# Optimization experiments

Hardware: AMD Instinct MI355X
Metric: run time of the kernel (lower is better)

## Reference

```python
import jax, jax.numpy as jnp
import numpy as np

CONTEXT_SIZE = 128
EMBED_DIM = 128
NUM_HEADS = 4
HEAD_SIZE = EMBED_DIM // NUM_HEADS  # 32


def setup_inputs() -> dict:
    key = jax.random.key(0)
    ks = jax.random.split(key, 9)
    B, T, D, H, hd = 4096, 128, EMBED_DIM, NUM_HEADS, HEAD_SIZE
    s = 1.0 / np.sqrt(D)
    return {
        "x": jax.random.normal(ks[0], (B, T, D), dtype=jnp.float32),
        "Wq": jax.random.normal(ks[1], (H, D, hd), dtype=jnp.float32) * s,
        "bq": jnp.zeros((H, hd), dtype=jnp.float32),
        "Wk": jax.random.normal(ks[2], (H, D, hd), dtype=jnp.float32) * s,
        "bk": jnp.zeros((H, hd), dtype=jnp.float32),
        "Wv": jax.random.normal(ks[3], (H, D, hd), dtype=jnp.float32) * s,
        "bv": jnp.zeros((H, hd), dtype=jnp.float32),
        "Wp": jax.random.normal(ks[4], (D, D), dtype=jnp.float32) * s,
        "bp": jnp.zeros((D,), dtype=jnp.float32),
    }


def reference(x, Wq, bq, Wk, bk, Wv, bv, Wp, bp):
    B, T, D = x.shape
    # per-head projections, batched over heads: [B,H,T,hd]
    q = jnp.einsum("btd,hdk->bhtk", x, Wq) + bq[None, :, None, :]
    k = jnp.einsum("btd,hdk->bhtk", x, Wk) + bk[None, :, None, :]
    v = jnp.einsum("btd,hdk->bhtk", x, Wv) + bv[None, :, None, :]
    # NOTE: original scales by context_size**-0.5, not head_size**-0.5
    scale = CONTEXT_SIZE ** (-0.5)
    scores = jnp.einsum("bhqk,bhsk->bhqs", q, k) * scale  # [B,H,T,T]
    causal = jnp.tril(jnp.ones((T, T), dtype=bool))
    scores = jnp.where(causal[None, None, :, :], scores, -jnp.inf)
    attn = jax.nn.softmax(scores, axis=-1)
    out = jnp.einsum("bhqs,bhsk->bhqk", attn, v)  # [B,H,T,hd]
    # concat heads along feature dim (head order matches ModuleList order)
    out = out.transpose(0, 2, 1, 3).reshape(B, T, D)
    # final projection; dropout is identity in eval mode
    return out @ Wp + bp
```

## Files before the change

kernel.cpp:

```cpp
#include <hip/hip_runtime.h>

#define NB 4096
#define T_ 128
#define D_ 128
#define H_ 4
#define HD_ 32

typedef __attribute__((ext_vector_type(8))) short short8;
typedef __attribute__((ext_vector_type(4))) float float4v;

__device__ inline unsigned short f2bf(float f) {
  unsigned int u = __builtin_bit_cast(unsigned int, f);
  u += 0x7fffu + ((u >> 16) & 1u);
  return (unsigned short)(u >> 16);
}


__global__ __launch_bounds__(512, 4) void mha_kernel(
    const float* __restrict__ x,  const float* __restrict__ Wq,
    const float* __restrict__ bq, const float* __restrict__ Wk,
    const float* __restrict__ bk, const float* __restrict__ Wv,
    const float* __restrict__ bv, const float* __restrict__ Wp,
    const float* __restrict__ bp, float* __restrict__ out)
{
  __shared__ __align__(16) unsigned short smem[32000];
  const int tid  = threadIdx.x;
  const int b    = blockIdx.x;
  const int wv_i = tid >> 6;
  const int lane = tid & 63;
  const int quad = lane >> 4;
  const int n16  = lane & 15;

  unsigned short* xs  = smem;
  unsigned short* osw = smem + wv_i * 2176;
  unsigned short* ks  = smem + 17408;
  unsigned short* wt  = smem + 22528;
  unsigned short* Ew  = smem + 26880 + wv_i * 640;
  unsigned short* wpT = smem + 17408;

  const float4* x4 = (const float4*)(x + (size_t)b * 16384);
  #pragma unroll
  for (int i = 0; i < 8; ++i) {
    float4 v = x4[i * 512 + tid];
    int fl = (i * 512 + tid) * 4;
    xs[fl + 0] = f2bf(v.x); xs[fl + 1] = f2bf(v.y);
    xs[fl + 2] = f2bf(v.z); xs[fl + 3] = f2bf(v.w);
  }
  __syncthreads();

  short8 xfrag[4];
  {
    const unsigned short* base = xs + (wv_i * 16 + n16) * 128 + quad * 8;
    #pragma unroll
    for (int kk = 0; kk < 4; ++kk)
      xfrag[kk] = *(const short8*)(base + kk * 32);
  }
  __syncthreads();

  auto stageWT = [&](const float* Wsrc) {
    #pragma unroll
    for (int i = 0; i < 2; ++i) {
      int g4 = tid + i * 512;
      float4 v = ((const float4*)Wsrc)[g4];
      int g = g4 * 4; int d = g >> 5; int e = g & 31;
      wt[(e + 0) * 136 + d] = f2bf(v.x);
      wt[(e + 1) * 136 + d] = f2bf(v.y);
      wt[(e + 2) * 136 + d] = f2bf(v.z);
      wt[(e + 3) * 136 + d] = f2bf(v.w);
    }
  };

  auto projQKV = [&](float4v acc[2]) {
    #pragma unroll
    for (int nt = 0; nt < 2; ++nt) {
      acc[nt] = (float4v)(0.0f);
      #pragma unroll
      for (int kk = 0; kk < 4; ++kk) {
        short8 bfr = *(const short8*)(wt + (nt * 16 + n16) * 136 + kk * 32 + quad * 8);
        acc[nt] = __builtin_amdgcn_mfma_f32_16x16x32_bf16(xfrag[kk], bfr, acc[nt], 0, 0, 0);
      }
    }
  };

  const float LOG2E_SCALE = 0.08838834764831845f * 1.4426950408889634f;

  #pragma unroll 1
  for (int h = 0; h < H_; ++h) {
    __syncthreads();
    stageWT(Wk + h * 4096);
    __syncthreads();
    float4v kacc[2]; projQKV(kacc);
    #pragma unroll
    for (int nt = 0; nt < 2; ++nt) {
      float bias = bk[h * 32 + nt * 16 + n16];
      #pragma unroll
      for (int r = 0; r < 4; ++r)
        ks[(wv_i * 16 + quad * 4 + r) * 40 + nt * 16 + n16] = f2bf(kacc[nt][r] + bias);
    }
    __syncthreads();
    stageWT(Wq + h * 4096);
    __syncthreads();
    float4v qacc[2]; projQKV(qacc);
    #pragma unroll
    for (int nt = 0; nt < 2; ++nt) {
      float bias = bq[h * 32 + nt * 16 + n16];
      #pragma unroll
      for (int r = 0; r < 4; ++r)
        Ew[(quad * 4 + r) * 40 + nt * 16 + n16] = f2bf(qacc[nt][r] + bias);
    }
    short8 qfrag = *(const short8*)(Ew + n16 * 40 + quad * 8);
    __syncthreads();
    stageWT(Wv + h * 4096);
    __syncthreads();
    float4v vacc[2]; projQKV(vacc);
    __syncthreads();
    #pragma unroll
    for (int nt = 0; nt < 2; ++nt) {
      float bias = bv[h * 32 + nt * 16 + n16];
      #pragma unroll
      for (int r = 0; r < 4; ++r)
        wt[(nt * 16 + n16) * 136 + wv_i * 16 + quad * 4 + r] = f2bf(vacc[nt][r] + bias);
    }
    __syncthreads();

    float4v s[8];
    #pragma unroll
    for (int t = 0; t < 8; ++t) {
      if (t <= wv_i) {
        short8 kfr = *(const short8*)(ks + (t * 16 + n16) * 40 + quad * 8);
        float4v acc = __builtin_amdgcn_mfma_f32_16x16x32_bf16(qfrag, kfr, (float4v)(0.0f), 0, 0, 0);
        if (t == wv_i) {
          #pragma unroll
          for (int r = 0; r < 4; ++r)
            if (n16 > quad * 4 + r) acc[r] = -__builtin_inff();
        }
        s[t] = acc;
      }
    }

    float l[4];
    #pragma unroll
    for (int r = 0; r < 4; ++r) {
      float mm = -__builtin_inff();
      #pragma unroll
      for (int t = 0; t < 8; ++t) if (t <= wv_i) mm = fmaxf(mm, s[t][r]);
      #pragma unroll
      for (int off = 8; off >= 1; off >>= 1) mm = fmaxf(mm, __shfl_xor(mm, off, 64));
      float ll = 0.0f;
      #pragma unroll
      for (int t = 0; t < 8; ++t) if (t <= wv_i) {
        float p = exp2f((s[t][r] - mm) * LOG2E_SCALE);
        s[t][r] = p; ll += p;
      }
      #pragma unroll
      for (int off = 8; off >= 1; off >>= 1) ll += __shfl_xor(ll, off, 64);
      l[r] = ll;
    }

    float4v oacc[2] = {(float4v)(0.0f), (float4v)(0.0f)};
    #pragma unroll
    for (int c = 0; c < 4; ++c) {
      if (2 * c <= wv_i) {
        #pragma unroll
        for (int tt = 0; tt < 2; ++tt) {
          int t = 2 * c + tt;
          #pragma unroll
          for (int r = 0; r < 4; ++r)
            Ew[(quad * 4 + r) * 40 + tt * 16 + n16] =
                (t <= wv_i) ? f2bf(s[t][r]) : (unsigned short)0;
        }
        short8 pfrag = *(const short8*)(Ew + n16 * 40 + quad * 8);
        #pragma unroll
        for (int et = 0; et < 2; ++et) {
          short8 vfr = *(const short8*)(wt + (et * 16 + n16) * 136 + c * 32 + quad * 8);
          oacc[et] = __builtin_amdgcn_mfma_f32_16x16x32_bf16(pfrag, vfr, oacc[et], 0, 0, 0);
        }
      }
    }
    #pragma unroll
    for (int et = 0; et < 2; ++et) {
      #pragma unroll
      for (int r = 0; r < 4; ++r)
        osw[(quad * 4 + r) * 136 + h * 32 + et * 16 + n16] = f2bf(oacc[et][r] / l[r]);
    }
  }

  short8 ofrag[4];
  #pragma unroll
  for (int kk = 0; kk < 4; ++kk)
    ofrag[kk] = *(const short8*)(osw + n16 * 136 + kk * 32 + quad * 8);
  float* outb = out + (size_t)b * 16384;

  #pragma unroll 1
  for (int half = 0; half < 2; ++half) {
    __syncthreads();
    #pragma unroll
    for (int i = 0; i < 4; ++i) {
      int g4 = tid + i * 512;
      int g = g4 * 4; int c = g >> 6; int dd = g & 63;
      float4 v = *(const float4*)(Wp + c * 128 + half * 64 + dd);
      wpT[(dd + 0) * 136 + c] = f2bf(v.x);
      wpT[(dd + 1) * 136 + c] = f2bf(v.y);
      wpT[(dd + 2) * 136 + c] = f2bf(v.z);
      wpT[(dd + 3) * 136 + c] = f2bf(v.w);
    }
    __syncthreads();
    #pragma unroll
    for (int nt = 0; nt < 4; ++nt) {
      float4v acc = (float4v)(0.0f);
      #pragma unroll
      for (int kk = 0; kk < 4; ++kk) {
        short8 bfr = *(const short8*)(wpT + (nt * 16 + n16) * 136 + kk * 32 + quad * 8);
        acc = __builtin_amdgcn_mfma_f32_16x16x32_bf16(ofrag[kk], bfr, acc, 0, 0, 0);
      }
      int col = half * 64 + nt * 16 + n16;
      float bias = bp[col];
      #pragma unroll
      for (int r = 0; r < 4; ++r)
        outb[(size_t)(wv_i * 16 + quad * 4 + r) * 128 + col] = acc[r] + bias;
    }
  }
}

extern "C" void kernel_launch(void* const* d_in, const int* in_sizes, int n_in,
                              void* d_out, int out_size, void* d_ws, size_t ws_size,
                              hipStream_t stream) {
  const float* x  = (const float*)d_in[0];
  const float* Wq = (const float*)d_in[1];
  const float* bq = (const float*)d_in[2];
  const float* Wk = (const float*)d_in[3];
  const float* bk = (const float*)d_in[4];
  const float* Wv = (const float*)d_in[5];
  const float* bv = (const float*)d_in[6];
  const float* Wp = (const float*)d_in[7];
  const float* bp = (const float*)d_in[8];
  mha_kernel<<<dim3(NB), dim3(512), 0, stream>>>(
      x, Wq, bq, Wk, bk, Wv, bv, Wp, bp, (float*)d_out);
}
```

Before: 719.7 us.

## Pre-convert weights to bf16 once and read MFMA operands directly from global

A small prep kernel converts and transposes Wq/Wk/Wv/Wp to bf16 in the workspace once per call. The main kernel then loads weight MFMA fragments straight from global/L2 instead of restaging and transposing fp32 weights through LDS in every block. x fragments are loaded directly into registers, and the per-head syncs collapse from five to two. LDS use drops from 64KB to about 29KB, which may allow more blocks per CU, at the cost of an extra launch and uncached-looking global fragment loads.

```diff
diff --git a/kernel.cpp b/kernel.cpp
--- a/kernel.cpp
+++ b/kernel.cpp
@@ -1,12 +1,9 @@
 #include <hip/hip_runtime.h>
 
 #define NB 4096
-#define T_ 128
-#define D_ 128
-#define H_ 4
-#define HD_ 32
 
 typedef __attribute__((ext_vector_type(8))) short short8;
+typedef __attribute__((ext_vector_type(4))) short short4v;
 typedef __attribute__((ext_vector_type(4))) float float4v;
 
 __device__ inline unsigned short f2bf(float f) {
@@ -15,15 +12,32 @@
   return (unsigned short)(u >> 16);
 }
 
+__global__ __launch_bounds__(256) void prep_weights(
+    const float* __restrict__ Wq, const float* __restrict__ Wk,
+    const float* __restrict__ Wv, const float* __restrict__ Wp,
+    unsigned short* __restrict__ ws)
+{
+  int idx = blockIdx.x * 256 + threadIdx.x;
+  if (idx < 49152) {
+    int m = idx >> 14;
+    int r = idx & 16383;
+    int h = r >> 12, e = (r >> 7) & 31, d = r & 127;
+    const float* W = (m == 0) ? Wq : (m == 1) ? Wk : Wv;
+    ws[idx] = f2bf(W[h * 4096 + d * 32 + e]);
+  } else if (idx < 65536) {
+    int r = idx - 49152;
+    int col = r >> 7, d = r & 127;
+    ws[idx] = f2bf(Wp[d * 128 + col]);
+  }
+}
 
 __global__ __launch_bounds__(512, 4) void mha_kernel(
-    const float* __restrict__ x,  const float* __restrict__ Wq,
-    const float* __restrict__ bq, const float* __restrict__ Wk,
-    const float* __restrict__ bk, const float* __restrict__ Wv,
-    const float* __restrict__ bv, const float* __restrict__ Wp,
-    const float* __restrict__ bp, float* __restrict__ out)
+    const float* __restrict__ x, const unsigned short* __restrict__ wbf,
+    const float* __restrict__ bq, const float* __restrict__ bk,
+    const float* __restrict__ bv, const float* __restrict__ bp,
+    float* __restrict__ out)
 {
-  __shared__ __align__(16) unsigned short smem[32000];
+  __shared__ __align__(16) unsigned short smem[14592];
   const int tid  = threadIdx.x;
   const int b    = blockIdx.x;
   const int wv_i = tid >> 6;
@@ -31,65 +45,54 @@
   const int quad = lane >> 4;
   const int n16  = lane & 15;
 
-  unsigned short* xs  = smem;
-  unsigned short* osw = smem + wv_i * 2176;
-  unsigned short* ks  = smem + 17408;
-  unsigned short* wt  = smem + 22528;
-  unsigned short* Ew  = smem + 26880 + wv_i * 640;
-  unsigned short* wpT = smem + 17408;
-
-  const float4* x4 = (const float4*)(x + (size_t)b * 16384);
+  unsigned short* ks = smem;
+  unsigned short* vt = smem + 5120;
+  unsigned short* Ew = smem + 9472 + wv_i * 640;
+
+  const unsigned short* wq  = wbf;
+  const unsigned short* wk  = wbf + 16384;
+  const unsigned short* wvw = wbf + 32768;
+  const unsigned short* wpT = wbf + 49152;
+
+  const float* xrow = x + (size_t)b * 16384 + (wv_i * 16 + n16) * 128 + quad * 8;
+  short8 xfrag[4];
   #pragma unroll
-  for (int i = 0; i < 8; ++i) {
-    float4 v = x4[i * 512 + tid];
-    int fl = (i * 512 + tid) * 4;
-    xs[fl + 0] = f2bf(v.x); xs[fl + 1] = f2bf(v.y);
-    xs[fl + 2] = f2bf(v.z); xs[fl + 3] = f2bf(v.w);
-  }
-  __syncthreads();
-
-  short8 xfrag[4];
-  {
-    const unsigned short* base = xs + (wv_i * 16 + n16) * 128 + quad * 8;
-    #pragma unroll
-    for (int kk = 0; kk < 4; ++kk)
-      xfrag[kk] = *(const short8*)(base + kk * 32);
-  }
-  __syncthreads();
-
-  auto stageWT = [&](const float* Wsrc) {
-    #pragma unroll
-    for (int i = 0; i < 2; ++i) {
-      int g4 = tid + i * 512;
-      float4 v = ((const float4*)Wsrc)[g4];
-      int g = g4 * 4; int d = g >> 5; int e = g & 31;
-      wt[(e + 0) * 136 + d] = f2bf(v.x);
-      wt[(e + 1) * 136 + d] = f2bf(v.y);
-      wt[(e + 2) * 136 + d] = f2bf(v.z);
-      wt[(e + 3) * 136 + d] = f2bf(v.w);
+  for (int kk = 0; kk < 4; ++kk) {
+    float4 a = *(const float4*)(xrow + kk * 32);
+    float4 c = *(const float4*)(xrow + kk * 32 + 4);
+    short8 f;
+    f[0] = (short)f2bf(a.x); f[1] = (short)f2bf(a.y);
+    f[2] = (short)f2bf(a.z); f[3] = (short)f2bf(a.w);
+    f[4] = (short)f2bf(c.x); f[5] = (short)f2bf(c.y);
+    f[6] = (short)f2bf(c.z); f[7] = (short)f2bf(c.w);
+    xfrag[kk] = f;
+  }
+
+  auto projQKV = [&](const unsigned short* wm, float4v acc[2]) {
+    #pragma unroll
+    for (int nt = 0; nt < 2; ++nt) {
+      acc[nt] = (float4v)(0.0f);
+      #pragma unroll
+      for (int kk = 0; kk < 4; ++kk) {
+        short8 bfr = *(const short8*)(wm + (nt * 16 + n16) * 128 + kk * 32 + quad * 8);
+        acc[nt] = __builtin_amdgcn_mfma_f32_16x16x32_bf16(xfrag[kk], bfr, acc[nt], 0, 0, 0);
+      }
     }
   };
 
-  auto projQKV = [&](float4v acc[2]) {
-    #pragma unroll
-    for (int nt = 0; nt < 2; ++nt) {
-      acc[nt] = (float4v)(0.0f);
-      #pragma unroll
-      for (int kk = 0; kk < 4; ++kk) {
-        short8 bfr = *(const short8*)(wt + (nt * 16 + n16) * 136 + kk * 32 + quad * 8);
-        acc[nt] = __builtin_amdgcn_mfma_f32_16x16x32_bf16(xfrag[kk], bfr, acc[nt], 0, 0, 0);
-      }
-    }
-  };
-
   const float LOG2E_SCALE = 0.08838834764831845f * 1.4426950408889634f;
 
+  short8 ofrag0, ofrag1, ofrag2, ofrag3;
+
   #pragma unroll 1
-  for (int h = 0; h < H_; ++h) {
+  for (int h = 0; h < 4; ++h) {
+    float4v kacc[2], qacc[2], vacc[2];
+    projQKV(wk  + h * 4096, kacc);
+    projQKV(wq  + h * 4096, qacc);
+    projQKV(wvw + h * 4096, vacc);
+
     __syncthreads();
-    stageWT(Wk + h * 4096);
-    __syncthreads();
-    float4v kacc[2]; projQKV(kacc);
+
     #pragma unroll
     for (int nt = 0; nt < 2; ++nt) {
       float bias = bk[h * 32 + nt * 16 + n16];
@@ -97,10 +100,14 @@
       for (int r = 0; r < 4; ++r)
         ks[(wv_i * 16 + quad * 4 + r) * 40 + nt * 16 + n16] = f2bf(kacc[nt][r] + bias);
     }
-    __syncthreads();
-    stageWT(Wq + h * 4096);
-    __syncthreads();
-    float4v qacc[2]; projQKV(qacc);
+    #pragma unroll
+    for (int nt = 0; nt < 2; ++nt) {
+      float bias = bv[h * 32 + nt * 16 + n16];
+      short4v p;
+      #pragma unroll
+      for (int r = 0; r < 4; ++r) p[r] = (short)f2bf(vacc[nt][r] + bias);
+      *(short4v*)(vt + (nt * 16 + n16) * 136 + wv_i * 16 + quad * 4) = p;
+    }
     #pragma unroll
     for (int nt = 0; nt < 2; ++nt) {
       float bias = bq[h * 32 + nt * 16 + n16];
@@ -109,18 +116,7 @@
         Ew[(quad * 4 + r) * 40 + nt * 16 + n16] = f2bf(qacc[nt][r] + bias);
     }
     short8 qfrag = *(const short8*)(Ew + n16 * 40 + quad * 8);
-    __syncthreads();
-    stageWT(Wv + h * 4096);
-    __syncthreads();
-    float4v vacc[2]; projQKV(vacc);
-    __syncthreads();
-    #pragma unroll
-    for (int nt = 0; nt < 2; ++nt) {
-      float bias = bv[h * 32 + nt * 16 + n16];
-      #pragma unroll
-      for (int r = 0; r < 4; ++r)
-        wt[(nt * 16 + n16) * 136 + wv_i * 16 + quad * 4 + r] = f2bf(vacc[nt][r] + bias);
-    }
+
     __syncthreads();
 
     float4v s[8];
@@ -172,52 +168,42 @@
         short8 pfrag = *(const short8*)(Ew + n16 * 40 + quad * 8);
         #pragma unroll
         for (int et = 0; et < 2; ++et) {
-          short8 vfr = *(const short8*)(wt + (et * 16 + n16) * 136 + c * 32 + quad * 8);
+          short8 vfr = *(const short8*)(vt + (et * 16 + n16) * 136 + c * 32 + quad * 8);
           oacc[et] = __builtin_amdgcn_mfma_f32_16x16x32_bf16(pfrag, vfr, oacc[et], 0, 0, 0);
         }
       }
     }
+
+    float inv0 = 1.0f / l[0], inv1 = 1.0f / l[1], inv2 = 1.0f / l[2], inv3 = 1.0f / l[3];
     #pragma unroll
     for (int et = 0; et < 2; ++et) {
+      Ew[(quad * 4 + 0) * 40 + et * 16 + n16] = f2bf(oacc[et][0] * inv0);
+      Ew[(quad * 4 + 1) * 40 + et * 16 + n16] = f2bf(oacc[et][1] * inv1);
+      Ew[(quad * 4 + 2) * 40 + et * 16 + n16] = f2bf(oacc[et][2] * inv2);
+      Ew[(quad * 4 + 3) * 40 + et * 16 + n16] = f2bf(oacc[et][3] * inv3);
+    }
+    short8 of = *(const short8*)(Ew + n16 * 40 + quad * 8);
+    if (h == 0) ofrag0 = of; else if (h == 1) ofrag1 = of;
+    else if (h == 2) ofrag2 = of; else ofrag3 = of;
+  }
+
+  float* outb = out + (size_t)b * 16384;
+  const int row0 = wv_i * 16 + quad * 4;
+  #pragma unroll
+  for (int half = 0; half < 2; ++half) {
+    #pragma unroll
+    for (int nt = 0; nt < 4; ++nt) {
+      int col = half * 64 + nt * 16 + n16;
+      const unsigned short* wcol = wpT + col * 128 + quad * 8;
+      float4v acc = (float4v)(0.0f);
+      acc = __builtin_amdgcn_mfma_f32_16x16x32_bf16(ofrag0, *(const short8*)(wcol +  0), acc, 0, 0, 0);
+      acc = __builtin_amdgcn_mfma_f32_16x16x32_bf16(ofrag1, *(const short8*)(wcol + 32), acc, 0, 0, 0);
+      acc = __builtin_amdgcn_mfma_f32_16x16x32_bf16(ofrag2, *(const short8*)(wcol + 64), acc, 0, 0, 0);
+      acc = __builtin_amdgcn_mfma_f32_16x16x32_bf16(ofrag3, *(const short8*)(wcol + 96), acc, 0, 0, 0);
+      float bias = bp[col];
       #pragma unroll
       for (int r = 0; r < 4; ++r)
-        osw[(quad * 4 + r) * 136 + h * 32 + et * 16 + n16] = f2bf(oacc[et][r] / l[r]);
-    }
-  }
-
-  short8 ofrag[4];
-  #pragma unroll
-  for (int kk = 0; kk < 4; ++kk)
-    ofrag[kk] = *(const short8*)(osw + n16 * 136 + kk * 32 + quad * 8);
-  float* outb = out + (size_t)b * 16384;
-
-  #pragma unroll 1
-  for (int half = 0; half < 2; ++half) {
-    __syncthreads();
-    #pragma unroll
-    for (int i = 0; i < 4; ++i) {
-      int g4 = tid + i * 512;
-      int g = g4 * 4; int c = g >> 6; int dd = g & 63;
-      float4 v = *(const float4*)(Wp + c * 128 + half * 64 + dd);
-      wpT[(dd + 0) * 136 + c] = f2bf(v.x);
-      wpT[(dd + 1) * 136 + c] = f2bf(v.y);
-      wpT[(dd + 2) * 136 + c] = f2bf(v.z);
-      wpT[(dd + 3) * 136 + c] = f2bf(v.w);
-    }
-    __syncthreads();
-    #pragma unroll
-    for (int nt = 0; nt < 4; ++nt) {
-      float4v acc = (float4v)(0.0f);
-      #pragma unroll
-      for (int kk = 0; kk < 4; ++kk) {
-        short8 bfr = *(const short8*)(wpT + (nt * 16 + n16) * 136 + kk * 32 + quad * 8);
-        acc = __builtin_amdgcn_mfma_f32_16x16x32_bf16(ofrag[kk], bfr, acc, 0, 0, 0);
-      }
-      int col = half * 64 + nt * 16 + n16;
-      float bias = bp[col];
-      #pragma unroll
-      for (int r = 0; r < 4; ++r)
-        outb[(size_t)(wv_i * 16 + quad * 4 + r) * 128 + col] = acc[r] + bias;
+        outb[(size_t)(row0 + r) * 128 + col] = acc[r] + bias;
     }
   }
 }
@@ -234,6 +220,7 @@
   const float* bv = (const float*)d_in[6];
   const float* Wp = (const float*)d_in[7];
   const float* bp = (const float*)d_in[8];
-  mha_kernel<<<dim3(NB), dim3(512), 0, stream>>>(
-      x, Wq, bq, Wk, bk, Wv, bv, Wp, bp, (float*)d_out);
-}
+  unsigned short* ws = (unsigned short*)d_ws;
+  prep_weights<<<dim3(256), dim3(256), 0, stream>>>(Wq, Wk, Wv, Wp, ws);
+  mha_kernel<<<dim3(NB), dim3(512), 0, stream>>>(x, ws, bq, bk, bv, bp, (float*)d_out);
+}
```

Result: slower. 935.8 us (+30.0%).
